# Kernel optimization log

Measured on AMD Instinct MI355X. Metric: run time of the kernel, lower is better.

The kernel has to match this reference:

```python
import jax, jax.numpy as jnp
import numpy as np
import math

D_MODEL = 512
N_HEADS = 8
HEAD_DIM = D_MODEL // N_HEADS


def setup_inputs() -> dict:
    key = jax.random.key(0)
    k1, k2, k3 = jax.random.split(key, 3)
    B, T = 2, 4096
    x = jax.random.normal(k1, (B, T, D_MODEL), dtype=jnp.float32)
    # nn.Linear weights: stored as [out, in], applied as x @ W.T
    W_QKV = jax.random.normal(k2, (3 * D_MODEL, D_MODEL), dtype=jnp.float32) * (1.0 / math.sqrt(D_MODEL))
    W_O = jax.random.normal(k3, (D_MODEL, D_MODEL), dtype=jnp.float32) * (1.0 / math.sqrt(D_MODEL))
    return {"x": x, "W_QKV": W_QKV, "W_O": W_O}


def reference(x, W_QKV, W_O):
    B, T, C = x.shape
    qkv = (x @ W_QKV.T).reshape(B, T, 3, N_HEADS, HEAD_DIM)
    q, k, v = qkv[:, :, 0], qkv[:, :, 1], qkv[:, :, 2]  # [B,T,H,D]
    # scores: [B,H,T,T]
    scale = math.sqrt(HEAD_DIM)
    attn = jnp.einsum('bqhd,bkhd->bhqk', q, k) / scale
    causal_mask = jnp.triu(jnp.ones((T, T), dtype=bool), k=1)
    attn = jnp.where(causal_mask, -jnp.inf, attn)
    attn = jax.nn.softmax(attn, axis=-1)
    out = jnp.einsum('bhqk,bkhd->bqhd', attn, v).reshape(B, T, C)
    return out @ W_O.T
```

## Files before the change

kernel.cpp:

```cpp
#include <hip/hip_runtime.h>
#include <hip/hip_bf16.h>

typedef __bf16 bf16_t;
typedef __bf16 bf16x8 __attribute__((ext_vector_type(8)));
typedef __bf16 bf16x4 __attribute__((ext_vector_type(4)));
typedef float  floatx4 __attribute__((ext_vector_type(4)));

static __device__ __forceinline__ floatx4 mfma16(bf16x8 a, bf16x8 b, floatx4 c) {
  return __builtin_amdgcn_mfma_f32_16x16x32_bf16(a, b, c, 0, 0, 0);
}

typedef __attribute__((address_space(3))) void lds_vp;
typedef __attribute__((address_space(1))) void glb_vp;
#define GLDS16(g, l) \
  __builtin_amdgcn_global_load_lds((glb_vp*)(g), (lds_vp*)(l), 16, 0, 0)

__global__ void cvt_all_kernel(const float* __restrict__ x,
                               const float* __restrict__ wqkv,
                               const float* __restrict__ wo,
                               bf16_t* __restrict__ xb,
                               bf16_t* __restrict__ wqkvb,
                               bf16_t* __restrict__ wob) {
  int i = blockIdx.x * blockDim.x + threadIdx.x;
  const float4* src; bf16x4* dst; int off;
  if (i < 1048576)      { src = (const float4*)x;    dst = (bf16x4*)xb;    off = i; }
  else if (i < 1245184) { src = (const float4*)wqkv; dst = (bf16x4*)wqkvb; off = i - 1048576; }
  else                  { src = (const float4*)wo;   dst = (bf16x4*)wob;   off = i - 1245184; }
  float4 v = src[off];
  bf16x4 o;
  o[0] = (bf16_t)v.x; o[1] = (bf16_t)v.y; o[2] = (bf16_t)v.z; o[3] = (bf16_t)v.w;
  dst[off] = o;
}

__global__ __launch_bounds__(256) void gemm_qkv(
    const bf16_t* __restrict__ A, const bf16_t* __restrict__ B,
    bf16_t* __restrict__ Qo, bf16_t* __restrict__ Ko, bf16_t* __restrict__ Vto)
{
  __shared__ __align__(16) bf16_t As[2][128 * 64];
  __shared__ __align__(16) bf16_t Bs[2][128 * 64];
  const int tid  = threadIdx.x;
  const int lane = tid & 63;
  const int w    = tid >> 6;
  const int quad = lane >> 4;
  const int l15  = lane & 15;
  const int l7   = lane & 7;
  const int wm   = w & 1;
  const int wn   = w >> 1;
  const int K    = 512;

  floatx4 acc[4][4];
  #pragma unroll
  for (int i = 0; i < 4; ++i)
    #pragma unroll
    for (int j = 0; j < 4; ++j)
      acc[i][j] = (floatx4){0.f, 0.f, 0.f, 0.f};

  const bf16_t* Ab = A + (size_t)blockIdx.x * 128 * K;
  const bf16_t* Bb = B + (size_t)blockIdx.y * 128 * K;

  auto stage = [&](int buf, int k0) {
    #pragma unroll
    for (int i = 0; i < 4; ++i) {
      int c = tid + 256 * i;
      int row = c >> 3, colc = c & 7;
      int gofs = ((colc ^ (row & 7)) << 3);
      GLDS16(&Ab[(size_t)row * K + k0 + gofs], &As[buf][c * 8]);
      GLDS16(&Bb[(size_t)row * K + k0 + gofs], &Bs[buf][c * 8]);
    }
  };

  stage(0, 0);
  for (int it = 0; it < 8; ++it) {
    const int cur = it & 1;
    __syncthreads();
    if (it + 1 < 8) stage(cur ^ 1, (it + 1) << 6);
    #pragma unroll
    for (int ks = 0; ks < 2; ++ks) {
      bf16x8 af[4], bfr[4];
      #pragma unroll
      for (int t = 0; t < 4; ++t) {
        af[t]  = *(const bf16x8*)&As[cur][(wm * 64 + t * 16 + l15) * 64 +
                                         (((ks * 4 + quad) ^ l7) << 3)];
        bfr[t] = *(const bf16x8*)&Bs[cur][(wn * 64 + t * 16 + l15) * 64 +
                                         (((ks * 4 + quad) ^ l7) << 3)];
      }
      #pragma unroll
      for (int mt = 0; mt < 4; ++mt)
        #pragma unroll
        for (int nt = 0; nt < 4; ++nt)
          acc[mt][nt] = mfma16(af[mt], bfr[nt], acc[mt][nt]);
    }
  }

  if (blockIdx.y < 8) {
    #pragma unroll
    for (int mt = 0; mt < 4; ++mt) {
      #pragma unroll
      for (int nt = 0; nt < 4; ++nt) {
        #pragma unroll
        for (int r = 0; r < 4; ++r) {
          int m = blockIdx.x * 128 + wm * 64 + mt * 16 + quad * 4 + r;
          int n = blockIdx.y * 128 + wn * 64 + nt * 16 + l15;
          float v = acc[mt][nt][r];
          int b = m >> 12, t = m & 4095;
          int h = (n >> 6) & 7, d = n & 63;
          size_t bh = (size_t)(b * 8 + h);
          if (n < 512)
            Qo[bh * 262144 + (size_t)t * 64 + d] = (bf16_t)(v * 0.18033688f);
          else
            Ko[bh * 262144 + (size_t)t * 64 + d] = (bf16_t)v;
        }
      }
    }
  } else {
    __syncthreads();
    bf16_t* L = &As[0][0];
    #pragma unroll
    for (int mt = 0; mt < 4; ++mt)
      #pragma unroll
      for (int nt = 0; nt < 4; ++nt) {
        int n_l = wn * 64 + nt * 16 + l15;
        int mc  = wm * 8 + mt * 2 + (quad >> 1);
        bf16x4 v4;
        #pragma unroll
        for (int r = 0; r < 4; ++r) v4[r] = (bf16_t)acc[mt][nt][r];
        *(bf16x4*)&L[n_l * 128 + ((mc ^ (n_l & 15)) << 3) + (quad & 1) * 4] = v4;
      }
    __syncthreads();
    const int t0 = (blockIdx.x & 31) * 128;
    const int b  = blockIdx.x >> 5;
    #pragma unroll
    for (int i = 0; i < 8; ++i) {
      int c = tid + 256 * i;
      int n_l = c >> 4, tc = c & 15;
      int h = ((blockIdx.y - 8) << 1) | (n_l >> 6);
      int d = n_l & 63;
      size_t bh = (size_t)(b * 8 + h);
      int base0 = (tc >> 2) * 32 + (tc & 3) * 4;
      bf16x4 lo = *(const bf16x4*)&L[n_l * 128 +
                     (((base0 >> 3) ^ (n_l & 15)) << 3) + (base0 & 7)];
      bf16x4 hi = *(const bf16x4*)&L[n_l * 128 +
                     ((((base0 + 16) >> 3) ^ (n_l & 15)) << 3) + (base0 & 7)];
      bf16x8 o;
      #pragma unroll
      for (int e = 0; e < 4; ++e) { o[e] = lo[e]; o[e + 4] = hi[e]; }
      *(bf16x8*)&Vto[bh * 262144 + (size_t)d * 4096 + t0 + tc * 8] = o;
    }
  }
}

__global__ __launch_bounds__(256) void gemm_out(
    const bf16_t* __restrict__ A, const bf16_t* __restrict__ B,
    float* __restrict__ Cf)
{
  __shared__ __align__(16) bf16_t As[2][64 * 64];
  __shared__ __align__(16) bf16_t Bs[2][128 * 64];
  const int tid  = threadIdx.x;
  const int lane = tid & 63;
  const int w    = tid >> 6;
  const int quad = lane >> 4;
  const int l15  = lane & 15;
  const int l7   = lane & 7;

  floatx4 acc[4][2];
  #pragma unroll
  for (int i = 0; i < 4; ++i)
    #pragma unroll
    for (int j = 0; j < 2; ++j)
      acc[i][j] = (floatx4){0.f, 0.f, 0.f, 0.f};

  const bf16_t* Ab = A + (size_t)blockIdx.x * 64 * 512;
  const bf16_t* Bb = B + (size_t)blockIdx.y * 128 * 512;

  auto stage = [&](int buf, int k0) {
    #pragma unroll
    for (int i = 0; i < 2; ++i) {
      int c = tid + 256 * i;
      int row = c >> 3, colc = c & 7;
      GLDS16(&Ab[(size_t)row * 512 + k0 + ((colc ^ (row & 7)) << 3)],
             &As[buf][c * 8]);
    }
    #pragma unroll
    for (int i = 0; i < 4; ++i) {
      int c = tid + 256 * i;
      int row = c >> 3, colc = c & 7;
      GLDS16(&Bb[(size_t)row * 512 + k0 + ((colc ^ (row & 7)) << 3)],
             &Bs[buf][c * 8]);
    }
  };

  stage(0, 0);
  for (int it = 0; it < 8; ++it) {
    const int cur = it & 1;
    __syncthreads();
    if (it + 1 < 8) stage(cur ^ 1, (it + 1) << 6);
    #pragma unroll
    for (int ks = 0; ks < 2; ++ks) {
      bf16x8 af[4], bfr[2];
      #pragma unroll
      for (int t = 0; t < 4; ++t)
        af[t]  = *(const bf16x8*)&As[cur][(t * 16 + l15) * 64 +
                                         (((ks * 4 + quad) ^ l7) << 3)];
      #pragma unroll
      for (int t = 0; t < 2; ++t)
        bfr[t] = *(const bf16x8*)&Bs[cur][(w * 32 + t * 16 + l15) * 64 +
                                         (((ks * 4 + quad) ^ l7) << 3)];
      #pragma unroll
      for (int mt = 0; mt < 4; ++mt)
        #pragma unroll
        for (int nt = 0; nt < 2; ++nt)
          acc[mt][nt] = mfma16(af[mt], bfr[nt], acc[mt][nt]);
    }
  }

  #pragma unroll
  for (int mt = 0; mt < 4; ++mt)
    #pragma unroll
    for (int nt = 0; nt < 2; ++nt)
      #pragma unroll
      for (int r = 0; r < 4; ++r) {
        int m = blockIdx.x * 64 + mt * 16 + quad * 4 + r;
        int n = blockIdx.y * 128 + w * 32 + nt * 16 + l15;
        Cf[(size_t)m * 512 + n] = acc[mt][nt][r];
      }
}

__global__ __launch_bounds__(512, 2) void attn_kernel(
    const bf16_t* __restrict__ Qg, const bf16_t* __restrict__ Kgl,
    const bf16_t* __restrict__ Vtg, bf16_t* __restrict__ Og)
{
  __shared__ __align__(16) bf16_t smem[49664];
  bf16_t* KsB  = smem;
  bf16_t* VtsB = smem + 16384;

  const int tid  = threadIdx.x;
  const int lane = tid & 63;
  const int w    = tid >> 6;
  const int tile = w >> 2;
  const int qh   = (w >> 1) & 1;
  const int kh   = w & 1;
  const int quad = lane >> 4;
  const int l15  = lane & 15;

  const int id = blockIdx.x;
  const int k8 = id & 7;
  const int j  = id >> 3;
  const int bh = 2 * k8 + (j & 1);
  const int x  = j >> 1;
  const int qtA = 31 - x, qtB = x;
  const int qt_g = tile ? qtB : qtA;
  const int qt2  = qt_g * 2 + qh;
  const size_t bh_off = (size_t)bh * 262144;
  const int b = bh >> 3, h = bh & 7;

  const int qbase = qt_g * 128 + qh * 64;
  bf16x8 aq0[4], aq1[4];
  #pragma unroll
  for (int qb = 0; qb < 4; ++qb) {
    const bf16_t* Qp = Qg + bh_off + (size_t)(qbase + qb * 16 + l15) * 64;
    aq0[qb] = *(const bf16x8*)&Qp[quad * 8];
    aq1[qb] = *(const bf16x8*)&Qp[32 + quad * 8];
  }
  bf16x8 ones;
  #pragma unroll
  for (int i = 0; i < 8; ++i) ones[i] = (bf16_t)1.0f;

  floatx4 acc_o[4][4], acc_l[4];
  #pragma unroll
  for (int qb = 0; qb < 4; ++qb) {
    #pragma unroll
    for (int dt = 0; dt < 4; ++dt) acc_o[qb][dt] = (floatx4){0.f, 0.f, 0.f, 0.f};
    acc_l[qb] = (floatx4){0.f, 0.f, 0.f, 0.f};
  }

  auto stage = [&](int buf, int kt) {
    const bf16_t* Kp = Kgl + bh_off + (size_t)kt * 8192;
    const bf16_t* Vp = Vtg + bh_off + (size_t)kt * 128;
    #pragma unroll
    for (int i = 0; i < 2; ++i) {
      int c = tid + 512 * i;
      int row = c >> 3, colc = c & 7;
      GLDS16(&Kp[row * 64 + ((colc ^ (row & 7)) << 3)], &KsB[buf * 8192 + c * 8]);
    }
    #pragma unroll
    for (int i = 0; i < 2; ++i) {
      int c = tid + 512 * i;
      int row = c >> 4, colc = c & 15;
      GLDS16(&Vp[(size_t)row * 4096 + ((colc ^ (row & 15)) << 3)],
             &VtsB[buf * 8192 + c * 8]);
    }
  };

  stage(0, 0);
  const int nkt = qtA + 1;
  const floatx4 z4 = (floatx4){0.f, 0.f, 0.f, 0.f};
  for (int kt = 0; kt < nkt; ++kt) {
    const int cur = kt & 1;
    __syncthreads();
    if (kt + 1 < nkt) stage(cur ^ 1, kt + 1);

    if (2 * kt + kh <= qt2) {
      const bf16_t* Kc = &KsB[cur * 8192 + kh * 64 * 64];
      const bf16_t* Vc = &VtsB[cur * 8192];
      floatx4 s[4][4];
      #pragma unroll
      for (int nt = 0; nt < 4; ++nt) {
        bf16x8 bk0 = *(const bf16x8*)&Kc[(nt * 16 + l15) * 64 +
                                         ((quad ^ (l15 & 7)) << 3)];
        s[0][nt] = mfma16(bk0, aq0[0], z4);
        s[1][nt] = mfma16(bk0, aq0[1], z4);
        s[2][nt] = mfma16(bk0, aq0[2], z4);
        s[3][nt] = mfma16(bk0, aq0[3], z4);
      }
      #pragma unroll
      for (int nt = 0; nt < 4; ++nt) {
        bf16x8 bk1 = *(const bf16x8*)&Kc[(nt * 16 + l15) * 64 +
                                         (((4 + quad) ^ (l15 & 7)) << 3)];
        #pragma unroll
        for (int qb = 0; qb < 4; ++qb)
          s[qb][nt] = mfma16(bk1, aq1[qb], s[qb][nt]);
      }

      if (2 * kt + kh == qt2) {
        #pragma unroll
        for (int qb = 0; qb < 4; ++qb)
          #pragma unroll
          for (int nt = 0; nt < 4; ++nt)
            #pragma unroll
            for (int r = 0; r < 4; ++r)
              if (nt * 16 + quad * 4 + r > qb * 16 + l15)
                s[qb][nt][r] = -3.0e38f;
      }
      #pragma unroll
      for (int qb = 0; qb < 4; ++qb)
        #pragma unroll
        for (int nt = 0; nt < 4; ++nt)
          #pragma unroll
          for (int r = 0; r < 4; ++r)
            s[qb][nt][r] = __builtin_amdgcn_exp2f(s[qb][nt][r]);

      #pragma unroll
      for (int kc = 0; kc < 2; ++kc) {
        bf16x8 pb[4];
        #pragma unroll
        for (int qb = 0; qb < 4; ++qb)
          #pragma unroll
          for (int r = 0; r < 4; ++r) {
            pb[qb][r]     = (bf16_t)s[qb][kc * 2][r];
            pb[qb][r + 4] = (bf16_t)s[qb][kc * 2 + 1][r];
          }
        #pragma unroll
        for (int qb = 0; qb < 4; ++qb)
          acc_l[qb] = mfma16(ones, pb[qb], acc_l[qb]);
        #pragma unroll
        for (int dt = 0; dt < 4; ++dt) {
          bf16x8 av = *(const bf16x8*)&Vc[(dt * 16 + l15) * 128 +
                         ((((kh * 2 + kc) * 4 + quad) ^ l15) << 3)];
          #pragma unroll
          for (int qb = 0; qb < 4; ++qb)
            acc_o[qb][dt] = mfma16(av, pb[qb], acc_o[qb][dt]);
        }
      }
    }
  }

  __syncthreads();
  float*  PART = (float*)smem;
  bf16_t* OUT  = smem + 33280;
  const int p = w >> 1;
  float* P = PART + p * 4160;

  if (kh == 1) {
    #pragma unroll
    for (int qb = 0; qb < 4; ++qb) {
      #pragma unroll
      for (int dt = 0; dt < 4; ++dt) {
        int chunk = (dt * 4 + quad) ^ l15;
        *(floatx4*)&P[(qb * 16 + l15) * 64 + chunk * 4] = acc_o[qb][dt];
      }
      if (quad == 0) P[4096 + qb * 16 + l15] = acc_l[qb][0];
    }
  }
  __syncthreads();
  if (kh == 0) {
    bf16_t* Ot = OUT + p * 4096;
    #pragma unroll
    for (int qb = 0; qb < 4; ++qb) {
      const int t_own = qb * 16 + l15;
      float rl = 1.0f / (acc_l[qb][0] + P[4096 + t_own]);
      #pragma unroll
      for (int dt = 0; dt < 4; ++dt) {
        int chunk = (dt * 4 + quad) ^ l15;
        floatx4 pp = *(const floatx4*)&P[t_own * 64 + chunk * 4];
        bf16x4 o4;
        #pragma unroll
        for (int r = 0; r < 4; ++r)
          o4[r] = (bf16_t)((acc_o[qb][dt][r] + pp[r]) * rl);
        *(bf16x4*)&Ot[t_own * 64 +
                      (((dt * 2 + (quad >> 1)) ^ (t_own & 7)) << 3) +
                      (quad & 1) * 4] = o4;
      }
    }
  }
  __syncthreads();
  {
    bf16_t* Ot = OUT + p * 4096;
    const int gtid = ((w & 1) << 6) | lane;
    #pragma unroll
    for (int i = 0; i < 4; ++i) {
      int cc = gtid + 128 * i;
      int t = cc >> 3, c = cc & 7;
      bf16x8 o8 = *(const bf16x8*)&Ot[t * 64 + ((c ^ (t & 7)) << 3)];
      int trow = qbase + t;
      *(bf16x8*)&Og[((size_t)b * 4096 + trow) * 512 + h * 64 + c * 8] = o8;
    }
  }
}

extern "C" void kernel_launch(void* const* d_in, const int* in_sizes, int n_in,
                              void* d_out, int out_size, void* d_ws, size_t ws_size,
                              hipStream_t stream) {
  const float* x    = (const float*)d_in[0];
  const float* wqkv = (const float*)d_in[1];
  const float* wo   = (const float*)d_in[2];
  float* out = (float*)d_out;

  char* ws = (char*)d_ws;
  bf16_t* xb    = (bf16_t*)(ws);
  bf16_t* wqkvb = (bf16_t*)(ws + 8388608);
  bf16_t* wob   = (bf16_t*)(ws + 9961472);
  bf16_t* Qb    = (bf16_t*)(ws + 10485760);
  bf16_t* Kb    = (bf16_t*)(ws + 18874368);
  bf16_t* Vtb   = (bf16_t*)(ws + 27262976);
  bf16_t* Ob    = xb;

  cvt_all_kernel<<<5120, 256, 0, stream>>>(x, wqkv, wo, xb, wqkvb, wob);

  gemm_qkv<<<dim3(64, 12), 256, 0, stream>>>(xb, wqkvb, Qb, Kb, Vtb);
  attn_kernel<<<dim3(256), 512, 0, stream>>>(Qb, Kb, Vtb, Ob);
  gemm_out<<<dim3(128, 4), 256, 0, stream>>>(Ob, wob, out);
}
```

Before: 147.4 us.

## Software-pipeline attention loop with triple buffering and sequential q-tile processing

Restructures the attention kernel so each block processes its two paired query tiles (qtA then qtB) one after another over a single flattened 33-step loop, rather than splitting warps across the two tiles concurrently. K/V staging becomes a three-deep ring of LDS buffers, and the QK^T/exp for step g+1 is interleaved with the PV accumulation for step g. The intent is to overlap the softmax and exp work with MFMA PV work and to balance the causal workload across warps. The cost is two sets of accumulators in registers, extra loop-control logic, and two epilogue passes.

```diff
diff --git a/kernel.cpp b/kernel.cpp
--- a/kernel.cpp
+++ b/kernel.cpp
@@ -229,192 +229,225 @@
     const bf16_t* __restrict__ Qg, const bf16_t* __restrict__ Kgl,
     const bf16_t* __restrict__ Vtg, bf16_t* __restrict__ Og)
 {
-  __shared__ __align__(16) bf16_t smem[49664];
-  bf16_t* KsB  = smem;
-  bf16_t* VtsB = smem + 16384;
+  __shared__ __align__(16) bf16_t smem[49152];
 
   const int tid  = threadIdx.x;
   const int lane = tid & 63;
   const int w    = tid >> 6;
-  const int tile = w >> 2;
-  const int qh   = (w >> 1) & 1;
+  const int qq   = w >> 1;
   const int kh   = w & 1;
   const int quad = lane >> 4;
   const int l15  = lane & 15;
+  const int qhb  = qq >> 1;
 
   const int id = blockIdx.x;
-  const int k8 = id & 7;
-  const int j  = id >> 3;
-  const int bh = 2 * k8 + (j & 1);
-  const int x  = j >> 1;
+  const int bh = 2 * (id & 7) + ((id >> 3) & 1);
+  const int x  = id >> 4;
   const int qtA = 31 - x, qtB = x;
-  const int qt_g = tile ? qtB : qtA;
-  const int qt2  = qt_g * 2 + qh;
   const size_t bh_off = (size_t)bh * 262144;
   const int b = bh >> 3, h = bh & 7;
 
-  const int qbase = qt_g * 128 + qh * 64;
-  bf16x8 aq0[4], aq1[4];
-  #pragma unroll
-  for (int qb = 0; qb < 4; ++qb) {
-    const bf16_t* Qp = Qg + bh_off + (size_t)(qbase + qb * 16 + l15) * 64;
-    aq0[qb] = *(const bf16x8*)&Qp[quad * 8];
-    aq1[qb] = *(const bf16x8*)&Qp[32 + quad * 8];
-  }
+  bf16x8 aq0[2], aq1[2];
+  auto loadQ = [&](int qt) {
+    #pragma unroll
+    for (int qb = 0; qb < 2; ++qb) {
+      const bf16_t* Qp = Qg + bh_off + (size_t)(qt * 128 + qq * 32 + qb * 16 + l15) * 64;
+      aq0[qb] = *(const bf16x8*)&Qp[quad * 8];
+      aq1[qb] = *(const bf16x8*)&Qp[32 + quad * 8];
+    }
+  };
+
   bf16x8 ones;
   #pragma unroll
   for (int i = 0; i < 8; ++i) ones[i] = (bf16_t)1.0f;
 
-  floatx4 acc_o[4][4], acc_l[4];
+  floatx4 accAo[2][4], accAl[2], accBo[2][4], accBl[2];
   #pragma unroll
-  for (int qb = 0; qb < 4; ++qb) {
-    #pragma unroll
-    for (int dt = 0; dt < 4; ++dt) acc_o[qb][dt] = (floatx4){0.f, 0.f, 0.f, 0.f};
-    acc_l[qb] = (floatx4){0.f, 0.f, 0.f, 0.f};
+  for (int qb = 0; qb < 2; ++qb) {
+    #pragma unroll
+    for (int dt = 0; dt < 4; ++dt) {
+      accAo[qb][dt] = (floatx4){0.f, 0.f, 0.f, 0.f};
+      accBo[qb][dt] = (floatx4){0.f, 0.f, 0.f, 0.f};
+    }
+    accAl[qb] = (floatx4){0.f, 0.f, 0.f, 0.f};
+    accBl[qb] = (floatx4){0.f, 0.f, 0.f, 0.f};
   }
 
-  auto stage = [&](int buf, int kt) {
+  auto stage = [&](int kB, int vB, int kt) {
     const bf16_t* Kp = Kgl + bh_off + (size_t)kt * 8192;
     const bf16_t* Vp = Vtg + bh_off + (size_t)kt * 128;
     #pragma unroll
     for (int i = 0; i < 2; ++i) {
       int c = tid + 512 * i;
       int row = c >> 3, colc = c & 7;
-      GLDS16(&Kp[row * 64 + ((colc ^ (row & 7)) << 3)], &KsB[buf * 8192 + c * 8]);
+      GLDS16(&Kp[row * 64 + ((colc ^ (row & 7)) << 3)], &smem[kB + c * 8]);
     }
     #pragma unroll
     for (int i = 0; i < 2; ++i) {
       int c = tid + 512 * i;
       int row = c >> 4, colc = c & 15;
-      GLDS16(&Vp[(size_t)row * 4096 + ((colc ^ (row & 15)) << 3)],
-             &VtsB[buf * 8192 + c * 8]);
-    }
-  };
-
-  stage(0, 0);
-  const int nkt = qtA + 1;
+      GLDS16(&Vp[(size_t)row * 4096 + ((colc ^ (row & 15)) << 3)], &smem[vB + c * 8]);
+    }
+  };
+
+  int kB0 = 0, kB1 = 8192, kB2 = 16384;
+  int vB0 = 24576, vB1 = 32768, vB2 = 40960;
+
+  floatx4 s2[2][4];
+  bf16x8 pb[2][2];
   const floatx4 z4 = (floatx4){0.f, 0.f, 0.f, 0.f};
-  for (int kt = 0; kt < nkt; ++kt) {
-    const int cur = kt & 1;
-    __syncthreads();
-    if (kt + 1 < nkt) stage(cur ^ 1, kt + 1);
-
-    if (2 * kt + kh <= qt2) {
-      const bf16_t* Kc = &KsB[cur * 8192 + kh * 64 * 64];
-      const bf16_t* Vc = &VtsB[cur * 8192];
-      floatx4 s[4][4];
-      #pragma unroll
-      for (int nt = 0; nt < 4; ++nt) {
-        bf16x8 bk0 = *(const bf16x8*)&Kc[(nt * 16 + l15) * 64 +
-                                         ((quad ^ (l15 & 7)) << 3)];
-        s[0][nt] = mfma16(bk0, aq0[0], z4);
-        s[1][nt] = mfma16(bk0, aq0[1], z4);
-        s[2][nt] = mfma16(bk0, aq0[2], z4);
-        s[3][nt] = mfma16(bk0, aq0[3], z4);
-      }
-      #pragma unroll
-      for (int nt = 0; nt < 4; ++nt) {
-        bf16x8 bk1 = *(const bf16x8*)&Kc[(nt * 16 + l15) * 64 +
-                                         (((4 + quad) ^ (l15 & 7)) << 3)];
-        #pragma unroll
-        for (int qb = 0; qb < 4; ++qb)
-          s[qb][nt] = mfma16(bk1, aq1[qb], s[qb][nt]);
-      }
-
-      if (2 * kt + kh == qt2) {
-        #pragma unroll
-        for (int qb = 0; qb < 4; ++qb)
-          #pragma unroll
-          for (int nt = 0; nt < 4; ++nt)
-            #pragma unroll
-            for (int r = 0; r < 4; ++r)
-              if (nt * 16 + quad * 4 + r > qb * 16 + l15)
-                s[qb][nt][r] = -3.0e38f;
-      }
-      #pragma unroll
-      for (int qb = 0; qb < 4; ++qb)
+
+  auto scompute = [&](int kB) {
+    #pragma unroll
+    for (int nt = 0; nt < 4; ++nt) {
+      bf16x8 bk = *(const bf16x8*)&smem[kB + (kh * 64 + nt * 16 + l15) * 64 +
+                                       ((quad ^ (l15 & 7)) << 3)];
+      s2[0][nt] = mfma16(bk, aq0[0], z4);
+      s2[1][nt] = mfma16(bk, aq0[1], z4);
+    }
+    #pragma unroll
+    for (int nt = 0; nt < 4; ++nt) {
+      bf16x8 bk = *(const bf16x8*)&smem[kB + (kh * 64 + nt * 16 + l15) * 64 +
+                                       (((4 + quad) ^ (l15 & 7)) << 3)];
+      s2[0][nt] = mfma16(bk, aq1[0], s2[0][nt]);
+      s2[1][nt] = mfma16(bk, aq1[1], s2[1][nt]);
+    }
+  };
+
+  auto exppack = [&](int diag) {
+    if (diag) {
+      #pragma unroll
+      for (int qb = 0; qb < 2; ++qb)
         #pragma unroll
         for (int nt = 0; nt < 4; ++nt)
           #pragma unroll
           for (int r = 0; r < 4; ++r)
-            s[qb][nt][r] = __builtin_amdgcn_exp2f(s[qb][nt][r]);
-
-      #pragma unroll
-      for (int kc = 0; kc < 2; ++kc) {
-        bf16x8 pb[4];
-        #pragma unroll
-        for (int qb = 0; qb < 4; ++qb)
+            if (nt * 16 + quad * 4 + r > (qq & 1) * 32 + qb * 16 + l15)
+              s2[qb][nt][r] = -3.0e38f;
+    }
+    #pragma unroll
+    for (int qb = 0; qb < 2; ++qb)
+      #pragma unroll
+      for (int nt = 0; nt < 4; ++nt)
+        #pragma unroll
+        for (int r = 0; r < 4; ++r)
+          s2[qb][nt][r] = __builtin_amdgcn_exp2f(s2[qb][nt][r]);
+    #pragma unroll
+    for (int qb = 0; qb < 2; ++qb)
+      #pragma unroll
+      for (int kc = 0; kc < 2; ++kc)
+        #pragma unroll
+        for (int r = 0; r < 4; ++r) {
+          pb[qb][kc][r]     = (bf16_t)s2[qb][kc * 2][r];
+          pb[qb][kc][r + 4] = (bf16_t)s2[qb][kc * 2 + 1][r];
+        }
+  };
+
+#define PV_STEP(ao, al, vB)                                                   \
+  do {                                                                        \
+    _Pragma("unroll")                                                         \
+    for (int kc = 0; kc < 2; ++kc) {                                          \
+      al[0] = mfma16(ones, pb[0][kc], al[0]);                                 \
+      al[1] = mfma16(ones, pb[1][kc], al[1]);                                 \
+      _Pragma("unroll")                                                       \
+      for (int dt = 0; dt < 4; ++dt) {                                        \
+        bf16x8 av = *(const bf16x8*)&smem[(vB) + (dt * 16 + l15) * 128 +      \
+                       ((((kh * 2 + kc) * 4 + quad) ^ l15) << 3)];            \
+        ao[0][dt] = mfma16(av, pb[0][kc], ao[0][dt]);                         \
+        ao[1][dt] = mfma16(av, pb[1][kc], ao[1][dt]);                         \
+      }                                                                       \
+    }                                                                         \
+  } while (0)
+
+  loadQ(qtA);
+  stage(kB0, vB0, 0);
+  stage(kB1, vB1, 1);
+  __syncthreads();
+  scompute(kB0);
+  exppack(0);
+
+  for (int g = 0; g < 33; ++g) {
+    if (g <= 30) {
+      int s = g + 2;
+      int kts = (s <= qtA) ? s : s - qtA - 1;
+      stage(kB2, vB2, kts);
+    }
+    int act1 = 0, diag1 = 0;
+    if (g <= 31) {
+      if (g == qtA) loadQ(qtB);
+      int s1 = g + 1;
+      int qt1 = (s1 <= qtA) ? qtA : qtB;
+      int kt1 = (s1 <= qtA) ? s1 : s1 - qtA - 1;
+      int kb2 = 2 * kt1 + kh, qb2 = 2 * qt1 + qhb;
+      act1 = (kb2 <= qb2);
+      diag1 = (kb2 == qb2);
+      if (act1) scompute(kB1);
+    }
+    {
+      int qt0 = (g <= qtA) ? qtA : qtB;
+      int kt0 = (g <= qtA) ? g : g - qtA - 1;
+      if (2 * kt0 + kh <= 2 * qt0 + qhb) {
+        if (g <= qtA) { PV_STEP(accAo, accAl, vB0); }
+        else          { PV_STEP(accBo, accBl, vB0); }
+      }
+    }
+    if (act1) exppack(diag1);
+    __syncthreads();
+    int t;
+    t = kB0; kB0 = kB1; kB1 = kB2; kB2 = t;
+    t = vB0; vB0 = vB1; vB1 = vB2; vB2 = t;
+  }
+#undef PV_STEP
+
+  auto epi = [&](int qt_e, floatx4 (&ao)[2][4], floatx4 (&al)[2]) {
+    float*  PART = (float*)smem;
+    float*  PL   = (float*)smem + 8192;
+    bf16_t* OUT  = smem + 16640;
+    __syncthreads();
+    if (kh == 1) {
+      #pragma unroll
+      for (int qb = 0; qb < 2; ++qb) {
+        int t_own = qq * 32 + qb * 16 + l15;
+        #pragma unroll
+        for (int dt = 0; dt < 4; ++dt) {
+          int chunk = (dt * 4 + quad) ^ l15;
+          *(floatx4*)&PART[t_own * 64 + chunk * 4] = ao[qb][dt];
+        }
+        if (quad == 0) PL[t_own] = al[qb][0];
+      }
+    }
+    __syncthreads();
+    if (kh == 0) {
+      #pragma unroll
+      for (int qb = 0; qb < 2; ++qb) {
+        int t_own = qq * 32 + qb * 16 + l15;
+        float rl = 1.0f / (al[qb][0] + PL[t_own]);
+        #pragma unroll
+        for (int dt = 0; dt < 4; ++dt) {
+          int chunk = (dt * 4 + quad) ^ l15;
+          floatx4 pp = *(const floatx4*)&PART[t_own * 64 + chunk * 4];
+          bf16x4 o4;
           #pragma unroll
-          for (int r = 0; r < 4; ++r) {
-            pb[qb][r]     = (bf16_t)s[qb][kc * 2][r];
-            pb[qb][r + 4] = (bf16_t)s[qb][kc * 2 + 1][r];
-          }
-        #pragma unroll
-        for (int qb = 0; qb < 4; ++qb)
-          acc_l[qb] = mfma16(ones, pb[qb], acc_l[qb]);
-        #pragma unroll
-        for (int dt = 0; dt < 4; ++dt) {
-          bf16x8 av = *(const bf16x8*)&Vc[(dt * 16 + l15) * 128 +
-                         ((((kh * 2 + kc) * 4 + quad) ^ l15) << 3)];
-          #pragma unroll
-          for (int qb = 0; qb < 4; ++qb)
-            acc_o[qb][dt] = mfma16(av, pb[qb], acc_o[qb][dt]);
+          for (int r = 0; r < 4; ++r)
+            o4[r] = (bf16_t)((ao[qb][dt][r] + pp[r]) * rl);
+          *(bf16x4*)&OUT[t_own * 64 +
+                         (((dt * 2 + (quad >> 1)) ^ (t_own & 7)) << 3) +
+                         (quad & 1) * 4] = o4;
         }
       }
     }
-  }
-
-  __syncthreads();
-  float*  PART = (float*)smem;
-  bf16_t* OUT  = smem + 33280;
-  const int p = w >> 1;
-  float* P = PART + p * 4160;
-
-  if (kh == 1) {
-    #pragma unroll
-    for (int qb = 0; qb < 4; ++qb) {
-      #pragma unroll
-      for (int dt = 0; dt < 4; ++dt) {
-        int chunk = (dt * 4 + quad) ^ l15;
-        *(floatx4*)&P[(qb * 16 + l15) * 64 + chunk * 4] = acc_o[qb][dt];
-      }
-      if (quad == 0) P[4096 + qb * 16 + l15] = acc_l[qb][0];
-    }
-  }
-  __syncthreads();
-  if (kh == 0) {
-    bf16_t* Ot = OUT + p * 4096;
-    #pragma unroll
-    for (int qb = 0; qb < 4; ++qb) {
-      const int t_own = qb * 16 + l15;
-      float rl = 1.0f / (acc_l[qb][0] + P[4096 + t_own]);
-      #pragma unroll
-      for (int dt = 0; dt < 4; ++dt) {
-        int chunk = (dt * 4 + quad) ^ l15;
-        floatx4 pp = *(const floatx4*)&P[t_own * 64 + chunk * 4];
-        bf16x4 o4;
-        #pragma unroll
-        for (int r = 0; r < 4; ++r)
-          o4[r] = (bf16_t)((acc_o[qb][dt][r] + pp[r]) * rl);
-        *(bf16x4*)&Ot[t_own * 64 +
-                      (((dt * 2 + (quad >> 1)) ^ (t_own & 7)) << 3) +
-                      (quad & 1) * 4] = o4;
-      }
-    }
-  }
-  __syncthreads();
-  {
-    bf16_t* Ot = OUT + p * 4096;
-    const int gtid = ((w & 1) << 6) | lane;
-    #pragma unroll
-    for (int i = 0; i < 4; ++i) {
-      int cc = gtid + 128 * i;
+    __syncthreads();
+    #pragma unroll
+    for (int i = 0; i < 2; ++i) {
+      int cc = tid + 512 * i;
       int t = cc >> 3, c = cc & 7;
-      bf16x8 o8 = *(const bf16x8*)&Ot[t * 64 + ((c ^ (t & 7)) << 3)];
-      int trow = qbase + t;
+      bf16x8 o8 = *(const bf16x8*)&OUT[t * 64 + ((c ^ (t & 7)) << 3)];
+      int trow = qt_e * 128 + t;
       *(bf16x8*)&Og[((size_t)b * 4096 + trow) * 512 + h * 64 + c * 8] = o8;
     }
-  }
+  };
+  epi(qtA, accAo, accAl);
+  epi(qtB, accBo, accBl);
 }
 
 extern "C" void kernel_launch(void* const* d_in, const int* in_sizes, int n_in,
```

Result: slower. 162.6 us (+10.3%).

## Split attention block over four key slices and process paired query tiles sequentially

Applied to the files above, without the earlier changes.

Before this change, each attention block ran two query tiles (one early, one late) in parallel across its wave groups, each split two ways over keys. Now the block handles the paired tiles one after the other, with all 8 waves on each tile: 2 query halves by 4 key-split waves, staging 256-key K/V tiles per step. The epilogue reduces four fp32 partials through LDS and writes bf16 output directly. The aim is to even out work, since the paired short and long tiles previously finished at different times, leaving waves idle. In exchange it uses more LDS, which may lower occupancy, and adds an extra reduction and synchronisation phase per tile.

```diff
diff --git a/kernel.cpp b/kernel.cpp
--- a/kernel.cpp
+++ b/kernel.cpp
@@ -229,191 +229,187 @@
     const bf16_t* __restrict__ Qg, const bf16_t* __restrict__ Kgl,
     const bf16_t* __restrict__ Vtg, bf16_t* __restrict__ Og)
 {
-  __shared__ __align__(16) bf16_t smem[49664];
-  bf16_t* KsB  = smem;
-  bf16_t* VtsB = smem + 16384;
+  __shared__ __align__(16) bf16_t smem[66560];
 
   const int tid  = threadIdx.x;
   const int lane = tid & 63;
   const int w    = tid >> 6;
-  const int tile = w >> 2;
-  const int qh   = (w >> 1) & 1;
-  const int kh   = w & 1;
+  const int qh   = w >> 2;
+  const int ks   = w & 3;
   const int quad = lane >> 4;
   const int l15  = lane & 15;
+  const int l7   = lane & 7;
 
   const int id = blockIdx.x;
-  const int k8 = id & 7;
-  const int j  = id >> 3;
-  const int bh = 2 * k8 + (j & 1);
-  const int x  = j >> 1;
+  const int bh = 2 * (id & 7) + ((id >> 3) & 1);
+  const int x  = id >> 4;
   const int qtA = 31 - x, qtB = x;
-  const int qt_g = tile ? qtB : qtA;
-  const int qt2  = qt_g * 2 + qh;
   const size_t bh_off = (size_t)bh * 262144;
   const int b = bh >> 3, h = bh & 7;
 
-  const int qbase = qt_g * 128 + qh * 64;
   bf16x8 aq0[4], aq1[4];
-  #pragma unroll
-  for (int qb = 0; qb < 4; ++qb) {
-    const bf16_t* Qp = Qg + bh_off + (size_t)(qbase + qb * 16 + l15) * 64;
-    aq0[qb] = *(const bf16x8*)&Qp[quad * 8];
-    aq1[qb] = *(const bf16x8*)&Qp[32 + quad * 8];
-  }
+  auto loadQ = [&](int qt) {
+    #pragma unroll
+    for (int qb = 0; qb < 4; ++qb) {
+      const bf16_t* Qp = Qg + bh_off +
+                         (size_t)(qt * 128 + qh * 64 + qb * 16 + l15) * 64;
+      aq0[qb] = *(const bf16x8*)&Qp[quad * 8];
+      aq1[qb] = *(const bf16x8*)&Qp[32 + quad * 8];
+    }
+  };
+
   bf16x8 ones;
   #pragma unroll
   for (int i = 0; i < 8; ++i) ones[i] = (bf16_t)1.0f;
 
   floatx4 acc_o[4][4], acc_l[4];
-  #pragma unroll
-  for (int qb = 0; qb < 4; ++qb) {
-    #pragma unroll
-    for (int dt = 0; dt < 4; ++dt) acc_o[qb][dt] = (floatx4){0.f, 0.f, 0.f, 0.f};
-    acc_l[qb] = (floatx4){0.f, 0.f, 0.f, 0.f};
-  }
-
-  auto stage = [&](int buf, int kt) {
-    const bf16_t* Kp = Kgl + bh_off + (size_t)kt * 8192;
-    const bf16_t* Vp = Vtg + bh_off + (size_t)kt * 128;
+  auto zacc = [&]() {
+    #pragma unroll
+    for (int qb = 0; qb < 4; ++qb) {
+      #pragma unroll
+      for (int dt = 0; dt < 4; ++dt) acc_o[qb][dt] = (floatx4){0.f, 0.f, 0.f, 0.f};
+      acc_l[qb] = (floatx4){0.f, 0.f, 0.f, 0.f};
+    }
+  };
+
+  auto stage = [&](int buf, int j) {
+    const bf16_t* Kp = Kgl + bh_off + (size_t)j * 16384;
+    const bf16_t* Vp = Vtg + bh_off + (size_t)j * 256;
+    const int base = buf * 32768;
+    #pragma unroll
+    for (int i = 0; i < 4; ++i) {
+      int c = tid + 512 * i;
+      int row = c >> 3, p = c & 7;
+      GLDS16(&Kp[(size_t)row * 64 + ((p ^ (row & 7)) << 3)], &smem[base + c * 8]);
+    }
+    #pragma unroll
+    for (int i = 0; i < 4; ++i) {
+      int c = tid + 512 * i;
+      int row = c >> 5, p = c & 31;
+      GLDS16(&Vp[(size_t)row * 4096 + ((p ^ (row & 15)) << 3)],
+             &smem[base + 16384 + c * 8]);
+    }
+  };
+
+  auto epi = [&](int qt) {
+    __syncthreads();
+    {
+      float* Pq = (float*)&smem[0] + qh * 16384 + ks * 4096;
+      float* PL = (float*)&smem[65536];
+      #pragma unroll
+      for (int qb = 0; qb < 4; ++qb) {
+        int q = qb * 16 + l15;
+        #pragma unroll
+        for (int dt = 0; dt < 4; ++dt)
+          *(floatx4*)&Pq[q * 64 + (((dt * 4 + quad) ^ l15) << 2)] = acc_o[qb][dt];
+        if (quad == 0) PL[qh * 256 + ks * 64 + q] = acc_l[qb][0];
+      }
+    }
+    __syncthreads();
     #pragma unroll
     for (int i = 0; i < 2; ++i) {
-      int c = tid + 512 * i;
-      int row = c >> 3, colc = c & 7;
-      GLDS16(&Kp[row * 64 + ((colc ^ (row & 7)) << 3)], &KsB[buf * 8192 + c * 8]);
-    }
-    #pragma unroll
-    for (int i = 0; i < 2; ++i) {
-      int c = tid + 512 * i;
-      int row = c >> 4, colc = c & 15;
-      GLDS16(&Vp[(size_t)row * 4096 + ((colc ^ (row & 15)) << 3)],
-             &VtsB[buf * 8192 + c * 8]);
-    }
-  };
-
-  stage(0, 0);
-  const int nkt = qtA + 1;
+      int a = tid + 512 * i;
+      int qh_e = a >> 9, rem = a & 511;
+      int q = rem >> 3, c8 = rem & 7;
+      const float* Pq = (const float*)&smem[0] + qh_e * 16384;
+      const float* PL = (const float*)&smem[65536] + qh_e * 256;
+      float s0[8] = {0.f, 0.f, 0.f, 0.f, 0.f, 0.f, 0.f, 0.f};
+      float suml = 0.f;
+      #pragma unroll
+      for (int k2 = 0; k2 < 4; ++k2) {
+        const float* Pk = Pq + k2 * 4096 + q * 64;
+        floatx4 u0 = *(const floatx4*)&Pk[((c8 * 2)     ^ (q & 15)) << 2];
+        floatx4 u1 = *(const floatx4*)&Pk[((c8 * 2 + 1) ^ (q & 15)) << 2];
+        #pragma unroll
+        for (int r = 0; r < 4; ++r) { s0[r] += u0[r]; s0[4 + r] += u1[r]; }
+        suml += PL[k2 * 64 + q];
+      }
+      float rl = 1.0f / suml;
+      bf16x8 o;
+      #pragma unroll
+      for (int e = 0; e < 8; ++e) o[e] = (bf16_t)(s0[e] * rl);
+      int row = qt * 128 + qh_e * 64 + q;
+      *(bf16x8*)&Og[((size_t)b * 4096 + row) * 512 + h * 64 + c8 * 8] = o;
+    }
+  };
+
   const floatx4 z4 = (floatx4){0.f, 0.f, 0.f, 0.f};
-  for (int kt = 0; kt < nkt; ++kt) {
-    const int cur = kt & 1;
-    __syncthreads();
-    if (kt + 1 < nkt) stage(cur ^ 1, kt + 1);
-
-    if (2 * kt + kh <= qt2) {
-      const bf16_t* Kc = &KsB[cur * 8192 + kh * 64 * 64];
-      const bf16_t* Vc = &VtsB[cur * 8192];
-      floatx4 s[4][4];
-      #pragma unroll
-      for (int nt = 0; nt < 4; ++nt) {
-        bf16x8 bk0 = *(const bf16x8*)&Kc[(nt * 16 + l15) * 64 +
-                                         ((quad ^ (l15 & 7)) << 3)];
-        s[0][nt] = mfma16(bk0, aq0[0], z4);
-        s[1][nt] = mfma16(bk0, aq0[1], z4);
-        s[2][nt] = mfma16(bk0, aq0[2], z4);
-        s[3][nt] = mfma16(bk0, aq0[3], z4);
-      }
-      #pragma unroll
-      for (int nt = 0; nt < 4; ++nt) {
-        bf16x8 bk1 = *(const bf16x8*)&Kc[(nt * 16 + l15) * 64 +
-                                         (((4 + quad) ^ (l15 & 7)) << 3)];
-        #pragma unroll
-        for (int qb = 0; qb < 4; ++qb)
-          s[qb][nt] = mfma16(bk1, aq1[qb], s[qb][nt]);
-      }
-
-      if (2 * kt + kh == qt2) {
+  for (int ph = 0; ph < 2; ++ph) {
+    const int qt = ph ? qtB : qtA;
+    if (ph) __syncthreads();
+    zacc();
+    loadQ(qt);
+    stage(0, 0);
+    const int N = (2 * qt + 5) >> 2;
+    const int lim = 2 * qt + qh;
+    for (int j = 0; j < N; ++j) {
+      const int cur = j & 1;
+      __syncthreads();
+      if (j + 1 < N) stage(cur ^ 1, j + 1);
+      const int kk = 4 * j + ks;
+      if (kk <= lim) {
+        const bf16_t* Kc = &smem[cur * 32768 + ks * 4096];
+        const bf16_t* Vc = &smem[cur * 32768 + 16384];
+        floatx4 s[4][4];
+        #pragma unroll
+        for (int nt = 0; nt < 4; ++nt) {
+          bf16x8 bk = *(const bf16x8*)&Kc[(nt * 16 + l15) * 64 +
+                                          ((quad ^ l7) << 3)];
+          s[0][nt] = mfma16(bk, aq0[0], z4);
+          s[1][nt] = mfma16(bk, aq0[1], z4);
+          s[2][nt] = mfma16(bk, aq0[2], z4);
+          s[3][nt] = mfma16(bk, aq0[3], z4);
+        }
+        #pragma unroll
+        for (int nt = 0; nt < 4; ++nt) {
+          bf16x8 bk = *(const bf16x8*)&Kc[(nt * 16 + l15) * 64 +
+                                          (((4 + quad) ^ l7) << 3)];
+          #pragma unroll
+          for (int qb = 0; qb < 4; ++qb)
+            s[qb][nt] = mfma16(bk, aq1[qb], s[qb][nt]);
+        }
+        if (kk == lim) {
+          #pragma unroll
+          for (int qb = 0; qb < 4; ++qb)
+            #pragma unroll
+            for (int nt = 0; nt < 4; ++nt)
+              #pragma unroll
+              for (int r = 0; r < 4; ++r)
+                if (nt * 16 + quad * 4 + r > qb * 16 + l15)
+                  s[qb][nt][r] = -3.0e38f;
+        }
         #pragma unroll
         for (int qb = 0; qb < 4; ++qb)
           #pragma unroll
           for (int nt = 0; nt < 4; ++nt)
             #pragma unroll
             for (int r = 0; r < 4; ++r)
-              if (nt * 16 + quad * 4 + r > qb * 16 + l15)
-                s[qb][nt][r] = -3.0e38f;
-      }
-      #pragma unroll
-      for (int qb = 0; qb < 4; ++qb)
-        #pragma unroll
-        for (int nt = 0; nt < 4; ++nt)
-          #pragma unroll
-          for (int r = 0; r < 4; ++r)
-            s[qb][nt][r] = __builtin_amdgcn_exp2f(s[qb][nt][r]);
-
-      #pragma unroll
-      for (int kc = 0; kc < 2; ++kc) {
-        bf16x8 pb[4];
-        #pragma unroll
-        for (int qb = 0; qb < 4; ++qb)
-          #pragma unroll
-          for (int r = 0; r < 4; ++r) {
-            pb[qb][r]     = (bf16_t)s[qb][kc * 2][r];
-            pb[qb][r + 4] = (bf16_t)s[qb][kc * 2 + 1][r];
+              s[qb][nt][r] = __builtin_amdgcn_exp2f(s[qb][nt][r]);
+        #pragma unroll
+        for (int kc = 0; kc < 2; ++kc) {
+          bf16x8 pb[4];
+          #pragma unroll
+          for (int qb = 0; qb < 4; ++qb)
+            #pragma unroll
+            for (int r = 0; r < 4; ++r) {
+              pb[qb][r]     = (bf16_t)s[qb][kc * 2][r];
+              pb[qb][r + 4] = (bf16_t)s[qb][kc * 2 + 1][r];
+            }
+          #pragma unroll
+          for (int qb = 0; qb < 4; ++qb)
+            acc_l[qb] = mfma16(ones, pb[qb], acc_l[qb]);
+          #pragma unroll
+          for (int dt = 0; dt < 4; ++dt) {
+            bf16x8 av = *(const bf16x8*)&Vc[(dt * 16 + l15) * 256 +
+                           ((((ks * 2 + kc) * 4 + quad) ^ l15) << 3)];
+            #pragma unroll
+            for (int qb = 0; qb < 4; ++qb)
+              acc_o[qb][dt] = mfma16(av, pb[qb], acc_o[qb][dt]);
           }
-        #pragma unroll
-        for (int qb = 0; qb < 4; ++qb)
-          acc_l[qb] = mfma16(ones, pb[qb], acc_l[qb]);
-        #pragma unroll
-        for (int dt = 0; dt < 4; ++dt) {
-          bf16x8 av = *(const bf16x8*)&Vc[(dt * 16 + l15) * 128 +
-                         ((((kh * 2 + kc) * 4 + quad) ^ l15) << 3)];
-          #pragma unroll
-          for (int qb = 0; qb < 4; ++qb)
-            acc_o[qb][dt] = mfma16(av, pb[qb], acc_o[qb][dt]);
         }
       }
     }
-  }
-
-  __syncthreads();
-  float*  PART = (float*)smem;
-  bf16_t* OUT  = smem + 33280;
-  const int p = w >> 1;
-  float* P = PART + p * 4160;
-
-  if (kh == 1) {
-    #pragma unroll
-    for (int qb = 0; qb < 4; ++qb) {
-      #pragma unroll
-      for (int dt = 0; dt < 4; ++dt) {
-        int chunk = (dt * 4 + quad) ^ l15;
-        *(floatx4*)&P[(qb * 16 + l15) * 64 + chunk * 4] = acc_o[qb][dt];
-      }
-      if (quad == 0) P[4096 + qb * 16 + l15] = acc_l[qb][0];
-    }
-  }
-  __syncthreads();
-  if (kh == 0) {
-    bf16_t* Ot = OUT + p * 4096;
-    #pragma unroll
-    for (int qb = 0; qb < 4; ++qb) {
-      const int t_own = qb * 16 + l15;
-      float rl = 1.0f / (acc_l[qb][0] + P[4096 + t_own]);
-      #pragma unroll
-      for (int dt = 0; dt < 4; ++dt) {
-        int chunk = (dt * 4 + quad) ^ l15;
-        floatx4 pp = *(const floatx4*)&P[t_own * 64 + chunk * 4];
-        bf16x4 o4;
-        #pragma unroll
-        for (int r = 0; r < 4; ++r)
-          o4[r] = (bf16_t)((acc_o[qb][dt][r] + pp[r]) * rl);
-        *(bf16x4*)&Ot[t_own * 64 +
-                      (((dt * 2 + (quad >> 1)) ^ (t_own & 7)) << 3) +
-                      (quad & 1) * 4] = o4;
-      }
-    }
-  }
-  __syncthreads();
-  {
-    bf16_t* Ot = OUT + p * 4096;
-    const int gtid = ((w & 1) << 6) | lane;
-    #pragma unroll
-    for (int i = 0; i < 4; ++i) {
-      int cc = gtid + 128 * i;
-      int t = cc >> 3, c = cc & 7;
-      bf16x8 o8 = *(const bf16x8*)&Ot[t * 64 + ((c ^ (t & 7)) << 3)];
-      int trow = qbase + t;
-      *(bf16x8*)&Og[((size_t)b * 4096 + trow) * 512 + h * 64 + c * 8] = o8;
-    }
+    epi(qt);
   }
 }
 
```

After: 153.9 us. 4.4% more time.

## Pre-swizzle K and V into MFMA fragment order and load directly from global

Applied to the files above, without the earlier changes.

The QKV GEMM now writes K and V in a blocked layout that matches the MFMA operand fragments, so each lane reads a contiguous 16-byte chunk. The attention kernel drops LDS staging, double buffering and the per-tile __syncthreads, and each wave loads its K/V fragments straight from global/L2 while walking its own 64-key chunks. This removes barrier and LDS traffic, but each wave now fetches K/V independently, relying on cache instead of shared reuse and exposing load latency without explicit prefetch. Launch bounds drop to one block per CU minimum, which allows more registers per thread.

```diff
diff --git a/kernel.cpp b/kernel.cpp
--- a/kernel.cpp
+++ b/kernel.cpp
@@ -108,7 +108,10 @@
           if (n < 512)
             Qo[bh * 262144 + (size_t)t * 64 + d] = (bf16_t)(v * 0.18033688f);
           else
-            Ko[bh * 262144 + (size_t)t * 64 + d] = (bf16_t)v;
+            Ko[bh * 262144 +
+               (size_t)((((t >> 4) * 2 + (d >> 5)) * 512) +
+                        ((((d & 31) >> 3) * 16 + (t & 15)) * 8) + (d & 7))] =
+                (bf16_t)v;
         }
       }
     }
@@ -144,7 +147,10 @@
       bf16x8 o;
       #pragma unroll
       for (int e = 0; e < 4; ++e) { o[e] = lo[e]; o[e + 4] = hi[e]; }
-      *(bf16x8*)&Vto[bh * 262144 + (size_t)d * 4096 + t0 + tc * 8] = o;
+      int T = t0 + tc * 8;
+      *(bf16x8*)&Vto[bh * 262144 +
+                     (size_t)((((T >> 5) * 4 + (d >> 4)) * 512) +
+                              ((((T >> 3) & 3) * 16 + (d & 15)) * 8))] = o;
     }
   }
 }
@@ -225,13 +231,11 @@
       }
 }
 
-__global__ __launch_bounds__(512, 2) void attn_kernel(
-    const bf16_t* __restrict__ Qg, const bf16_t* __restrict__ Kgl,
-    const bf16_t* __restrict__ Vtg, bf16_t* __restrict__ Og)
+__global__ __launch_bounds__(512, 1) void attn_kernel(
+    const bf16_t* __restrict__ Qg, const bf16_t* __restrict__ Kf,
+    const bf16_t* __restrict__ Vf, bf16_t* __restrict__ Og)
 {
   __shared__ __align__(16) bf16_t smem[49664];
-  bf16_t* KsB  = smem;
-  bf16_t* VtsB = smem + 16384;
 
   const int tid  = threadIdx.x;
   const int lane = tid & 63;
@@ -243,17 +247,15 @@
   const int l15  = lane & 15;
 
   const int id = blockIdx.x;
-  const int k8 = id & 7;
-  const int j  = id >> 3;
-  const int bh = 2 * k8 + (j & 1);
-  const int x  = j >> 1;
+  const int bh = 2 * (id & 7) + ((id >> 3) & 1);
+  const int x  = id >> 4;
   const int qtA = 31 - x, qtB = x;
-  const int qt_g = tile ? qtB : qtA;
-  const int qt2  = qt_g * 2 + qh;
+  const int qt  = tile ? qtB : qtA;
+  const int q64 = 2 * qt + qh;
   const size_t bh_off = (size_t)bh * 262144;
   const int b = bh >> 3, h = bh & 7;
 
-  const int qbase = qt_g * 128 + qh * 64;
+  const int qbase = qt * 128 + qh * 64;
   bf16x8 aq0[4], aq1[4];
   #pragma unroll
   for (int qb = 0; qb < 4; ++qb) {
@@ -273,94 +275,73 @@
     acc_l[qb] = (floatx4){0.f, 0.f, 0.f, 0.f};
   }
 
-  auto stage = [&](int buf, int kt) {
-    const bf16_t* Kp = Kgl + bh_off + (size_t)kt * 8192;
-    const bf16_t* Vp = Vtg + bh_off + (size_t)kt * 128;
-    #pragma unroll
-    for (int i = 0; i < 2; ++i) {
-      int c = tid + 512 * i;
-      int row = c >> 3, colc = c & 7;
-      GLDS16(&Kp[row * 64 + ((colc ^ (row & 7)) << 3)], &KsB[buf * 8192 + c * 8]);
-    }
-    #pragma unroll
-    for (int i = 0; i < 2; ++i) {
-      int c = tid + 512 * i;
-      int row = c >> 4, colc = c & 15;
-      GLDS16(&Vp[(size_t)row * 4096 + ((colc ^ (row & 15)) << 3)],
-             &VtsB[buf * 8192 + c * 8]);
-    }
-  };
-
-  stage(0, 0);
-  const int nkt = qtA + 1;
+  const bf16_t* Kb_ = Kf + bh_off;
+  const bf16_t* Vb_ = Vf + bh_off;
   const floatx4 z4 = (floatx4){0.f, 0.f, 0.f, 0.f};
-  for (int kt = 0; kt < nkt; ++kt) {
-    const int cur = kt & 1;
-    __syncthreads();
-    if (kt + 1 < nkt) stage(cur ^ 1, kt + 1);
-
-    if (2 * kt + kh <= qt2) {
-      const bf16_t* Kc = &KsB[cur * 8192 + kh * 64 * 64];
-      const bf16_t* Vc = &VtsB[cur * 8192];
-      floatx4 s[4][4];
-      #pragma unroll
-      for (int nt = 0; nt < 4; ++nt) {
-        bf16x8 bk0 = *(const bf16x8*)&Kc[(nt * 16 + l15) * 64 +
-                                         ((quad ^ (l15 & 7)) << 3)];
-        s[0][nt] = mfma16(bk0, aq0[0], z4);
-        s[1][nt] = mfma16(bk0, aq0[1], z4);
-        s[2][nt] = mfma16(bk0, aq0[2], z4);
-        s[3][nt] = mfma16(bk0, aq0[3], z4);
-      }
-      #pragma unroll
-      for (int nt = 0; nt < 4; ++nt) {
-        bf16x8 bk1 = *(const bf16x8*)&Kc[(nt * 16 + l15) * 64 +
-                                         (((4 + quad) ^ (l15 & 7)) << 3)];
-        #pragma unroll
-        for (int qb = 0; qb < 4; ++qb)
-          s[qb][nt] = mfma16(bk1, aq1[qb], s[qb][nt]);
-      }
-
-      if (2 * kt + kh == qt2) {
-        #pragma unroll
-        for (int qb = 0; qb < 4; ++qb)
-          #pragma unroll
-          for (int nt = 0; nt < 4; ++nt)
-            #pragma unroll
-            for (int r = 0; r < 4; ++r)
-              if (nt * 16 + quad * 4 + r > qb * 16 + l15)
-                s[qb][nt][r] = -3.0e38f;
-      }
+
+  for (int k64 = kh; k64 <= q64; k64 += 2) {
+    const bf16_t* Kp = Kb_ + (size_t)k64 * 4096;
+    const bf16_t* Vp = Vb_ + (size_t)k64 * 4096;
+    bf16x8 bk0[4], bk1[4];
+    #pragma unroll
+    for (int nt = 0; nt < 4; ++nt) {
+      bk0[nt] = *(const bf16x8*)&Kp[(nt * 2 + 0) * 512 + lane * 8];
+      bk1[nt] = *(const bf16x8*)&Kp[(nt * 2 + 1) * 512 + lane * 8];
+    }
+    floatx4 s[4][4];
+    #pragma unroll
+    for (int nt = 0; nt < 4; ++nt) {
+      s[0][nt] = mfma16(bk0[nt], aq0[0], z4);
+      s[1][nt] = mfma16(bk0[nt], aq0[1], z4);
+      s[2][nt] = mfma16(bk0[nt], aq0[2], z4);
+      s[3][nt] = mfma16(bk0[nt], aq0[3], z4);
+    }
+    #pragma unroll
+    for (int nt = 0; nt < 4; ++nt)
+      #pragma unroll
+      for (int qb = 0; qb < 4; ++qb)
+        s[qb][nt] = mfma16(bk1[nt], aq1[qb], s[qb][nt]);
+    bf16x8 av[2][4];
+    #pragma unroll
+    for (int kc = 0; kc < 2; ++kc)
+      #pragma unroll
+      for (int dt = 0; dt < 4; ++dt)
+        av[kc][dt] = *(const bf16x8*)&Vp[(kc * 4 + dt) * 512 + lane * 8];
+    if (k64 == q64) {
       #pragma unroll
       for (int qb = 0; qb < 4; ++qb)
         #pragma unroll
         for (int nt = 0; nt < 4; ++nt)
           #pragma unroll
           for (int r = 0; r < 4; ++r)
-            s[qb][nt][r] = __builtin_amdgcn_exp2f(s[qb][nt][r]);
-
-      #pragma unroll
-      for (int kc = 0; kc < 2; ++kc) {
-        bf16x8 pb[4];
+            if (nt * 16 + quad * 4 + r > qb * 16 + l15)
+              s[qb][nt][r] = -3.0e38f;
+    }
+    #pragma unroll
+    for (int qb = 0; qb < 4; ++qb)
+      #pragma unroll
+      for (int nt = 0; nt < 4; ++nt)
+        #pragma unroll
+        for (int r = 0; r < 4; ++r)
+          s[qb][nt][r] = __builtin_amdgcn_exp2f(s[qb][nt][r]);
+    #pragma unroll
+    for (int kc = 0; kc < 2; ++kc) {
+      bf16x8 pb[4];
+      #pragma unroll
+      for (int qb = 0; qb < 4; ++qb)
+        #pragma unroll
+        for (int r = 0; r < 4; ++r) {
+          pb[qb][r]     = (bf16_t)s[qb][kc * 2][r];
+          pb[qb][r + 4] = (bf16_t)s[qb][kc * 2 + 1][r];
+        }
+      #pragma unroll
+      for (int qb = 0; qb < 4; ++qb)
+        acc_l[qb] = mfma16(ones, pb[qb], acc_l[qb]);
+      #pragma unroll
+      for (int dt = 0; dt < 4; ++dt)
         #pragma unroll
         for (int qb = 0; qb < 4; ++qb)
-          #pragma unroll
-          for (int r = 0; r < 4; ++r) {
-            pb[qb][r]     = (bf16_t)s[qb][kc * 2][r];
-            pb[qb][r + 4] = (bf16_t)s[qb][kc * 2 + 1][r];
-          }
-        #pragma unroll
-        for (int qb = 0; qb < 4; ++qb)
-          acc_l[qb] = mfma16(ones, pb[qb], acc_l[qb]);
-        #pragma unroll
-        for (int dt = 0; dt < 4; ++dt) {
-          bf16x8 av = *(const bf16x8*)&Vc[(dt * 16 + l15) * 128 +
-                         ((((kh * 2 + kc) * 4 + quad) ^ l15) << 3)];
-          #pragma unroll
-          for (int qb = 0; qb < 4; ++qb)
-            acc_o[qb][dt] = mfma16(av, pb[qb], acc_o[qb][dt]);
-        }
-      }
+          acc_o[qb][dt] = mfma16(av[kc][dt], pb[qb], acc_o[qb][dt]);
     }
   }
 
@@ -430,13 +411,13 @@
   bf16_t* wqkvb = (bf16_t*)(ws + 8388608);
   bf16_t* wob   = (bf16_t*)(ws + 9961472);
   bf16_t* Qb    = (bf16_t*)(ws + 10485760);
-  bf16_t* Kb    = (bf16_t*)(ws + 18874368);
-  bf16_t* Vtb   = (bf16_t*)(ws + 27262976);
+  bf16_t* Kfb   = (bf16_t*)(ws + 18874368);
+  bf16_t* Vfb   = (bf16_t*)(ws + 27262976);
   bf16_t* Ob    = xb;
 
   cvt_all_kernel<<<5120, 256, 0, stream>>>(x, wqkv, wo, xb, wqkvb, wob);
 
-  gemm_qkv<<<dim3(64, 12), 256, 0, stream>>>(xb, wqkvb, Qb, Kb, Vtb);
-  attn_kernel<<<dim3(256), 512, 0, stream>>>(Qb, Kb, Vtb, Ob);
+  gemm_qkv<<<dim3(64, 12), 256, 0, stream>>>(xb, wqkvb, Qb, Kfb, Vfb);
+  attn_kernel<<<dim3(256), 512, 0, stream>>>(Qb, Kfb, Vfb, Ob);
   gemm_out<<<dim3(128, 4), 256, 0, stream>>>(Ob, wob, out);
 }
```

Result: no change. 148.1 us (+0.4%).
